# Performance work log

Hardware: AMD Instinct MI355X
Metric: run time of the kernel (lower is better)

## Reference

```python
import jax, jax.numpy as jnp
import numpy as np

BATCH, SEQ_LEN, D_MODEL = 8, 2048, 1024


def setup_inputs() -> dict:
    key = jax.random.key(0)
    ks = jax.random.split(key, 12)
    s = 0.02  # small init scale (stand-in for xavier)
    D, L = D_MODEL, SEQ_LEN
    return {
        "x": jax.random.normal(ks[0], (BATCH, L, D), jnp.float32),
        "W_B": jax.random.normal(ks[1], (D, D), jnp.float32) * s,
        "b_B": jnp.zeros((D,), jnp.float32),
        "W_C": jax.random.normal(ks[2], (D, D), jnp.float32) * s,
        "b_C": jnp.zeros((D,), jnp.float32),
        "W_d": jax.random.normal(ks[3], (D, D), jnp.float32) * s,
        "b_d": jnp.zeros((D,), jnp.float32),
        "delta_p": jax.random.normal(ks[4], (1, L, D), jnp.float32) * s,  # self.delta
        "A": jax.random.normal(ks[5], (L, D), jnp.float32) * s,
        "W_st": jax.random.normal(ks[6], (D, D), jnp.float32) * s,  # SToken fc1 Linear
        "b_st": jnp.zeros((D,), jnp.float32),
        "st_bias": jax.random.normal(ks[7], (1, 1, D), jnp.float32) * s,  # SToken bias
    }


def reference(x, W_B, b_B, W_C, b_C, W_d, b_d, delta_p, A, W_st, b_st, st_bias):
    # x: [B, L, D]
    z = jax.nn.sigmoid(x)
    B0 = x @ W_B.T + b_B          # LN_B(x)
    C = x @ W_C.T + b_C           # LN_C(x)

    # SToken: squeeze over seq, Linear -> ReLU -> Sigmoid, + bias, * x
    sq = jnp.mean(x, axis=1, keepdims=True)                    # [B, 1, D]
    sq = jax.nn.sigmoid(jax.nn.relu(sq @ W_st.T + b_st))
    T = (sq + st_bias) * x                                     # [B, L, D]

    delta = jax.nn.sigmoid(x @ W_d.T + b_d + delta_p)          # [B, L, D]
    A_ = delta * A                                             # broadcast [L, D]
    B_ = delta * B0

    # diagonal state-space recurrence: s_t = A_t * s_{t-1} + B_t * x_t; y_t = C_t * s_t + T_t
    def step(s, inputs):
        a_t, b_t, c_t, x_t, t_t = inputs                       # each [B, D]
        s = a_t * s + b_t * x_t
        y = c_t * s + t_t
        return s, y

    s0 = jnp.zeros((x.shape[0], x.shape[2]), x.dtype)
    xs = tuple(jnp.swapaxes(a, 0, 1) for a in (A_, B_, C, x, T))  # [L, B, D]
    _, ys = jax.lax.scan(step, s0, xs)
    x_out = jnp.swapaxes(ys, 0, 1) * z                         # [B, L, D]
    return x_out
```

## Files before the change

kernel.cpp:

```cpp
#include <hip/hip_runtime.h>
#include <hip/hip_bf16.h>
#include <cstdint>
#include <cstddef>

#define D_MODEL 1024
#define SEQ     2048
#define BATCH   8
#define M_TOT   (BATCH*SEQ)
#define N_TOT   (3*D_MODEL)
#define K_TOT   D_MODEL
#define KTILES  (K_TOT/64)
#define NCH     64
#define LCH     (SEQ/NCH)
#define W_UP    8

typedef unsigned short u16;
typedef __attribute__((ext_vector_type(8))) short short8;
typedef __attribute__((ext_vector_type(4))) float f32x4;

__device__ __forceinline__ u16 f2bf(float f) {
    __hip_bfloat16 h = __float2bfloat16(f);
    return __builtin_bit_cast(u16, h);
}
__device__ __forceinline__ uint packbf(float lo, float hi) {
    return (uint)f2bf(lo) | ((uint)f2bf(hi) << 16);
}
__device__ __forceinline__ float bf2f(u16 u) {
    __hip_bfloat16 h = __builtin_bit_cast(__hip_bfloat16, u);
    return __bfloat162float(h);
}
__device__ __forceinline__ float sigmoidf(float v) {
    return 1.0f / (1.0f + __expf(-v));
}
__device__ __forceinline__ void gld_lds16(const void* g, void* l) {
    __builtin_amdgcn_global_load_lds((const __attribute__((address_space(1))) void*)g,
                                     (__attribute__((address_space(3))) void*)l, 16, 0, 0);
}
__device__ __forceinline__ void wg_barrier() {
    asm volatile("" ::: "memory");
    __builtin_amdgcn_s_barrier();
    asm volatile("" ::: "memory");
}

__global__ void k_convert(const float* __restrict__ x, u16* __restrict__ xb,
                          float* __restrict__ sq,
                          const float* __restrict__ WB, const float* __restrict__ WC,
                          const float* __restrict__ Wd, u16* __restrict__ wcat,
                          const float* __restrict__ dp, const float* __restrict__ Aar,
                          uint2* __restrict__ dpA) {
    int bid = blockIdx.x;
    if (bid < 512) {
        int tblk = bid & 63, b = bid >> 6;
        int d = threadIdx.x * 4;
        size_t base = ((size_t)b * SEQ + (size_t)tblk * 32) * D_MODEL + d;
        float s0 = 0.f, s1 = 0.f, s2 = 0.f, s3 = 0.f;
        for (int t = 0; t < 32; ++t) {
            float4 v = *(const float4*)&x[base + (size_t)t * D_MODEL];
            s0 += v.x; s1 += v.y; s2 += v.z; s3 += v.w;
            ushort4 o = make_ushort4(f2bf(v.x), f2bf(v.y), f2bf(v.z), f2bf(v.w));
            *(ushort4*)&xb[base + (size_t)t * D_MODEL] = o;
        }
        atomicAdd(&sq[b * D_MODEL + d + 0], s0);
        atomicAdd(&sq[b * D_MODEL + d + 1], s1);
        atomicAdd(&sq[b * D_MODEL + d + 2], s2);
        atomicAdd(&sq[b * D_MODEL + d + 3], s3);
    } else if (bid < 3584) {
        int tg = (bid - 512) * 256 + threadIdx.x;
        size_t e0 = (size_t)tg * 4;
        int n = (int)(e0 >> 10), k0 = (int)(e0 & 1023);
        const float* W = (n < 1024) ? (WB + (size_t)n * 1024)
                       : (n < 2048) ? (WC + (size_t)(n - 1024) * 1024)
                                    : (Wd + (size_t)(n - 2048) * 1024);
        float4 v = *(const float4*)&W[k0];
        wcat[e0 + 0] = f2bf(v.x);
        wcat[e0 + 1] = f2bf(v.y);
        wcat[e0 + 2] = f2bf(v.z);
        wcat[e0 + 3] = f2bf(v.w);
    } else {
        int tg = (bid - 3584) * 256 + threadIdx.x;
        size_t e0 = (size_t)tg * 8;
        float4 d0 = *(const float4*)&dp[e0];
        float4 d1 = *(const float4*)&dp[e0 + 4];
        float4 a0 = *(const float4*)&Aar[e0];
        float4 a1 = *(const float4*)&Aar[e0 + 4];
        uint2* o = &dpA[e0 >> 1];
        o[0] = make_uint2(packbf(d0.x, d0.y), packbf(a0.x, a0.y));
        o[1] = make_uint2(packbf(d0.z, d0.w), packbf(a0.z, a0.w));
        o[2] = make_uint2(packbf(d1.x, d1.y), packbf(a1.x, a1.y));
        o[3] = make_uint2(packbf(d1.z, d1.w), packbf(a1.z, a1.w));
    }
}

__global__ void k_stoken(const float* __restrict__ sq, const float* __restrict__ Wst,
                         float* __restrict__ stacc) {
    __shared__ float s[BATCH][64];
    int nb = blockIdx.x & 3, ks = blockIdx.x >> 2;
    int k0 = ks * 64;
    for (int i = threadIdx.x; i < BATCH * 64; i += 256)
        s[i >> 6][i & 63] = sq[(i >> 6) * D_MODEL + k0 + (i & 63)] * (1.0f / SEQ);
    __syncthreads();
    int n = nb * 256 + threadIdx.x;
    const float* w = Wst + (size_t)n * D_MODEL + k0;
    float acc[BATCH] = {};
    for (int k = 0; k < 64; k += 4) {
        float4 wv = *(const float4*)&w[k];
#pragma unroll
        for (int b = 0; b < BATCH; ++b)
            acc[b] += s[b][k] * wv.x + s[b][k+1] * wv.y + s[b][k+2] * wv.z + s[b][k+3] * wv.w;
    }
#pragma unroll
    for (int b = 0; b < BATCH; ++b)
        atomicAdd(&stacc[b * D_MODEL + n], acc[b]);
}

#define HT_AL 0
#define HT_AH 1
#define HT_BL 2
#define HT_BH 3

__device__ __forceinline__ u16* ht_ptr(u16* ls, int buf, int which) {
    return ls + (size_t)(buf * 4 + which) * 8192;
}

__device__ __forceinline__ short8 ldsfrag2(const u16* ht, int R, int slot) {
    int off = R * 128 + ((slot ^ (R & 7)) << 4);
    return *(const short8*)((const char*)ht + off);
}

__device__ __forceinline__ void stage_half(const u16* __restrict__ S, u16* dst,
                                           int rowbase, int ktile, int w, int l) {
    int rsub = l >> 3;
    int scol = ((l & 7) ^ rsub) << 4;
    size_t kbyte = (size_t)ktile * 128;
#pragma unroll
    for (int j = 0; j < 2; ++j) {
        int s = 2 * w + j;
        int row = rowbase + s * 8 + rsub;
        gld_lds16((const char*)(S + (size_t)row * K_TOT) + kbyte + scol,
                  (char*)dst + s * 1024);
    }
}

template<bool SG, bool LAST>
__device__ __forceinline__ void kgroup4(const u16* __restrict__ A, const u16* __restrict__ Bm,
                                        u16* ls, int t, int i0, int n0,
                                        int wM, int wN, int r, int g, int w, int l,
                                        f32x4 acc[8][4]) {
    const int p = t & 1;
    u16* AL = ht_ptr(ls, p, HT_AL);
    u16* AH = ht_ptr(ls, p, HT_AH);
    u16* BL = ht_ptr(ls, p, HT_BL);
    u16* BH = ht_ptr(ls, p, HT_BH);
    u16* nAL = ht_ptr(ls, p ^ 1, HT_AL);
    u16* nAH = ht_ptr(ls, p ^ 1, HT_AH);
    u16* nBL = ht_ptr(ls, p ^ 1, HT_BL);
    u16* nBH = ht_ptr(ls, p ^ 1, HT_BH);
    const int RA = wM * 64 + r;
    const int RB = wN * 32 + r;

    short8 a[4][2], bl[2][2], bh[2][2];

#pragma unroll
    for (int m = 0; m < 4; ++m) {
        a[m][0] = ldsfrag2(AL, RA + m * 16, g);
        a[m][1] = ldsfrag2(AL, RA + m * 16, 4 + g);
    }
#pragma unroll
    for (int n = 0; n < 2; ++n) {
        bl[n][0] = ldsfrag2(BL, RB + n * 16, g);
        bl[n][1] = ldsfrag2(BL, RB + n * 16, 4 + g);
    }
    if (SG) stage_half(A, nAL, i0, t + 1, w, l);
    if (LAST) asm volatile("s_waitcnt vmcnt(0)" ::: "memory");
    else      asm volatile("s_waitcnt vmcnt(4)" ::: "memory");
    wg_barrier();
    __builtin_amdgcn_s_setprio(1);
#pragma unroll
    for (int m = 0; m < 4; ++m)
#pragma unroll
        for (int n = 0; n < 2; ++n)
            acc[m][n] = __builtin_amdgcn_mfma_f32_16x16x32_bf16(a[m][1], bl[n][1],
                        __builtin_amdgcn_mfma_f32_16x16x32_bf16(a[m][0], bl[n][0], acc[m][n], 0, 0, 0), 0, 0, 0);
    __builtin_amdgcn_s_setprio(0);

#pragma unroll
    for (int n = 0; n < 2; ++n) {
        bh[n][0] = ldsfrag2(BH, RB + n * 16, g);
        bh[n][1] = ldsfrag2(BH, RB + n * 16, 4 + g);
    }
    if (SG) stage_half(Bm, nBL, n0, t + 1, w, l);
    if (!LAST) asm volatile("s_waitcnt vmcnt(4)" ::: "memory");
    wg_barrier();
    __builtin_amdgcn_s_setprio(1);
#pragma unroll
    for (int m = 0; m < 4; ++m)
#pragma unroll
        for (int n = 0; n < 2; ++n)
            acc[m][2 + n] = __builtin_amdgcn_mfma_f32_16x16x32_bf16(a[m][1], bh[n][1],
                            __builtin_amdgcn_mfma_f32_16x16x32_bf16(a[m][0], bh[n][0], acc[m][2 + n], 0, 0, 0), 0, 0, 0);
    __builtin_amdgcn_s_setprio(0);

#pragma unroll
    for (int m = 0; m < 4; ++m) {
        a[m][0] = ldsfrag2(AH, RA + m * 16, g);
        a[m][1] = ldsfrag2(AH, RA + m * 16, 4 + g);
    }
    if (SG) stage_half(Bm, nBH, n0 + 128, t + 1, w, l);
    if (!LAST) asm volatile("s_waitcnt vmcnt(4)" ::: "memory");
    wg_barrier();
    __builtin_amdgcn_s_setprio(1);
#pragma unroll
    for (int m = 0; m < 4; ++m)
#pragma unroll
        for (int n = 0; n < 2; ++n)
            acc[4 + m][n] = __builtin_amdgcn_mfma_f32_16x16x32_bf16(a[m][1], bl[n][1],
                            __builtin_amdgcn_mfma_f32_16x16x32_bf16(a[m][0], bl[n][0], acc[4 + m][n], 0, 0, 0), 0, 0, 0);
    __builtin_amdgcn_s_setprio(0);

    if (SG) stage_half(A, nAH, i0 + 128, t + 1, w, l);
    if (!LAST) asm volatile("s_waitcnt vmcnt(4)" ::: "memory");
    wg_barrier();
    __builtin_amdgcn_s_setprio(1);
#pragma unroll
    for (int m = 0; m < 4; ++m)
#pragma unroll
        for (int n = 0; n < 2; ++n)
            acc[4 + m][2 + n] = __builtin_amdgcn_mfma_f32_16x16x32_bf16(a[m][1], bh[n][1],
                                __builtin_amdgcn_mfma_f32_16x16x32_bf16(a[m][0], bh[n][0], acc[4 + m][2 + n], 0, 0, 0), 0, 0, 0);
    __builtin_amdgcn_s_setprio(0);
}

__global__ __launch_bounds__(512, 2) void k_gemm(const u16* __restrict__ A,
                                                 const u16* __restrict__ Bm,
                                                 u16* __restrict__ Cout) {
    __shared__ u16 ls[8 * 8192];
    const int tid = threadIdx.x;
    const int l = tid & 63, w = tid >> 6;
    const int wM = w >> 2, wN = w & 3;
    const int r = l & 15, g = l >> 4;
    const int i0 = blockIdx.y * 256;
    const int n0 = blockIdx.x * 256;

    f32x4 acc[8][4] = {};

    stage_half(A,  ht_ptr(ls, 0, HT_AL), i0,       0, w, l);
    stage_half(Bm, ht_ptr(ls, 0, HT_BL), n0,       0, w, l);
    stage_half(Bm, ht_ptr(ls, 0, HT_BH), n0 + 128, 0, w, l);
    stage_half(A,  ht_ptr(ls, 0, HT_AH), i0 + 128, 0, w, l);
    asm volatile("s_waitcnt vmcnt(4)" ::: "memory");
    wg_barrier();

    for (int t = 0; t < KTILES - 1; ++t)
        kgroup4<true, false>(A, Bm, ls, t, i0, n0, wM, wN, r, g, w, l, acc);
    kgroup4<false, true>(A, Bm, ls, KTILES - 1, i0, n0, wM, wN, r, g, w, l, acc);

#pragma unroll
    for (int mi = 0; mi < 8; ++mi)
#pragma unroll
        for (int nj = 0; nj < 4; ++nj)
#pragma unroll
            for (int j = 0; j < 4; ++j) {
                size_t row = (size_t)(i0 + (mi >> 2) * 128 + wM * 64 + (mi & 3) * 16 + g * 4 + j);
                size_t col = (size_t)(n0 + (nj >> 1) * 128 + wN * 32 + (nj & 1) * 16 + r);
                Cout[row * N_TOT + col] = f2bf(acc[mi][nj][j]);
            }
}

__global__ void k_scan(const u16* __restrict__ xb, const u16* __restrict__ g3,
                       const uint2* __restrict__ dpA,
                       const float* __restrict__ bB, const float* __restrict__ bC,
                       const float* __restrict__ bd, const float* __restrict__ stacc,
                       const float* __restrict__ bst, const float* __restrict__ stb,
                       float* __restrict__ out) {
    int bid = blockIdx.x;
    int dblk = bid & 1, c = (bid >> 1) & (NCH - 1), b = bid >> 7;
    int d = dblk * 512 + threadIdx.x * 2;

    float2 bBv = *(const float2*)&bB[d];
    float2 bdv = *(const float2*)&bd[d];
    float2 bCv = *(const float2*)&bC[d];
    float2 sav = *(const float2*)&stacc[b * D_MODEL + d];
    float2 bstv = *(const float2*)&bst[d];
    float2 stbv = *(const float2*)&stb[d];
    float tc0 = sigmoidf(fmaxf(sav.x + bstv.x, 0.f)) + stbv.x;
    float tc1 = sigmoidf(fmaxf(sav.y + bstv.y, 0.f)) + stbv.y;

    int t0 = c * LCH;
    int tw = (c == 0) ? 0 : t0 - W_UP;
    float s0 = 0.f, s1 = 0.f;

    size_t xoff = ((size_t)b * SEQ + tw) * D_MODEL + d;
    size_t goff = ((size_t)b * SEQ + tw) * N_TOT + d;
    size_t ipa  = ((size_t)tw * D_MODEL + d) >> 1;

    for (int t = tw; t < t0; ++t) {
        uint xu = *(const uint*)&xb[xoff];
        uint gB = *(const uint*)&g3[goff];
        uint gd = *(const uint*)&g3[goff + 2048];
        uint2 pa = dpA[ipa];
        float x0 = bf2f((u16)(xu & 0xffff)), x1 = bf2f((u16)(xu >> 16));
        float b00 = bf2f((u16)(gB & 0xffff)) + bBv.x;
        float b01 = bf2f((u16)(gB >> 16)) + bBv.y;
        float de0 = sigmoidf(bf2f((u16)(gd & 0xffff)) + bdv.x + bf2f((u16)(pa.x & 0xffff)));
        float de1 = sigmoidf(bf2f((u16)(gd >> 16)) + bdv.y + bf2f((u16)(pa.x >> 16)));
        s0 = de0 * bf2f((u16)(pa.y & 0xffff)) * s0 + de0 * b00 * x0;
        s1 = de1 * bf2f((u16)(pa.y >> 16))    * s1 + de1 * b01 * x1;
        xoff += D_MODEL; goff += N_TOT; ipa += D_MODEL / 2;
    }
    for (int t = t0; t < t0 + LCH; ++t) {
        uint xu = *(const uint*)&xb[xoff];
        uint gB = *(const uint*)&g3[goff];
        uint gC = *(const uint*)&g3[goff + 1024];
        uint gd = *(const uint*)&g3[goff + 2048];
        uint2 pa = dpA[ipa];
        float x0 = bf2f((u16)(xu & 0xffff)), x1 = bf2f((u16)(xu >> 16));
        float b00 = bf2f((u16)(gB & 0xffff)) + bBv.x;
        float b01 = bf2f((u16)(gB >> 16)) + bBv.y;
        float de0 = sigmoidf(bf2f((u16)(gd & 0xffff)) + bdv.x + bf2f((u16)(pa.x & 0xffff)));
        float de1 = sigmoidf(bf2f((u16)(gd >> 16)) + bdv.y + bf2f((u16)(pa.x >> 16)));
        s0 = de0 * bf2f((u16)(pa.y & 0xffff)) * s0 + de0 * b00 * x0;
        s1 = de1 * bf2f((u16)(pa.y >> 16))    * s1 + de1 * b01 * x1;
        float c0 = bf2f((u16)(gC & 0xffff)) + bCv.x;
        float c1 = bf2f((u16)(gC >> 16)) + bCv.y;
        float y0 = (c0 * s0 + tc0 * x0) * sigmoidf(x0);
        float y1 = (c1 * s1 + tc1 * x1) * sigmoidf(x1);
        *(float2*)&out[xoff] = make_float2(y0, y1);
        xoff += D_MODEL; goff += N_TOT; ipa += D_MODEL / 2;
    }
}

extern "C" void kernel_launch(void* const* d_in, const int* in_sizes, int n_in,
                              void* d_out, int out_size, void* d_ws, size_t ws_size,
                              hipStream_t stream) {
    const float* x    = (const float*)d_in[0];
    const float* W_B  = (const float*)d_in[1];
    const float* b_B  = (const float*)d_in[2];
    const float* W_C  = (const float*)d_in[3];
    const float* b_C  = (const float*)d_in[4];
    const float* W_d  = (const float*)d_in[5];
    const float* b_d  = (const float*)d_in[6];
    const float* dp   = (const float*)d_in[7];
    const float* Aar  = (const float*)d_in[8];
    const float* W_st = (const float*)d_in[9];
    const float* b_st = (const float*)d_in[10];
    const float* stb  = (const float*)d_in[11];
    float* out = (float*)d_out;

    char* ws = (char*)d_ws;
    u16* xb    = (u16*)ws;   ws += (size_t)M_TOT * K_TOT * 2;
    u16* wcat  = (u16*)ws;   ws += (size_t)N_TOT * K_TOT * 2;
    u16* g3    = (u16*)ws;   ws += (size_t)M_TOT * N_TOT * 2;
    uint2* dpA = (uint2*)ws; ws += (size_t)SEQ * D_MODEL / 2 * 8;
    float* sq    = (float*)ws; ws += (size_t)BATCH * D_MODEL * 4;
    float* stacc = (float*)ws; ws += (size_t)BATCH * D_MODEL * 4;

    hipMemsetAsync(sq, 0, (size_t)2 * BATCH * D_MODEL * 4, stream);
    k_convert<<<4608, 256, 0, stream>>>(x, xb, sq, W_B, W_C, W_d, wcat, dp, Aar, dpA);
    k_stoken<<<64, 256, 0, stream>>>(sq, W_st, stacc);
    k_gemm<<<dim3(N_TOT / 256, M_TOT / 256), 512, 0, stream>>>(xb, wcat, g3);
    k_scan<<<1024, 256, 0, stream>>>(xb, g3, dpA, b_B, b_C, b_d,
                                     stacc, b_st, stb, out);
}
```

Measured before the change: 182.8 us.

## Fold SToken projection into GEMM launch and issue next-tile loads earlier

```diff
diff --git a/kernel.cpp b/kernel.cpp
--- a/kernel.cpp
+++ b/kernel.cpp
@@ -13,6 +13,7 @@
 #define NCH     64
 #define LCH     (SEQ/NCH)
 #define W_UP    8
+#define GEMM_BLKS (M_TOT/256 * N_TOT/256)
 
 typedef unsigned short u16;
 typedef __attribute__((ext_vector_type(8))) short short8;
@@ -91,28 +92,6 @@
     }
 }
 
-__global__ void k_stoken(const float* __restrict__ sq, const float* __restrict__ Wst,
-                         float* __restrict__ stacc) {
-    __shared__ float s[BATCH][64];
-    int nb = blockIdx.x & 3, ks = blockIdx.x >> 2;
-    int k0 = ks * 64;
-    for (int i = threadIdx.x; i < BATCH * 64; i += 256)
-        s[i >> 6][i & 63] = sq[(i >> 6) * D_MODEL + k0 + (i & 63)] * (1.0f / SEQ);
-    __syncthreads();
-    int n = nb * 256 + threadIdx.x;
-    const float* w = Wst + (size_t)n * D_MODEL + k0;
-    float acc[BATCH] = {};
-    for (int k = 0; k < 64; k += 4) {
-        float4 wv = *(const float4*)&w[k];
-#pragma unroll
-        for (int b = 0; b < BATCH; ++b)
-            acc[b] += s[b][k] * wv.x + s[b][k+1] * wv.y + s[b][k+2] * wv.z + s[b][k+3] * wv.w;
-    }
-#pragma unroll
-    for (int b = 0; b < BATCH; ++b)
-        atomicAdd(&stacc[b * D_MODEL + n], acc[b]);
-}
-
 #define HT_AL 0
 #define HT_AH 1
 #define HT_BL 2
@@ -160,6 +139,7 @@
 
     short8 a[4][2], bl[2][2], bh[2][2];
 
+    if (SG) stage_half(A, nAL, i0, t + 1, w, l);
 #pragma unroll
     for (int m = 0; m < 4; ++m) {
         a[m][0] = ldsfrag2(AL, RA + m * 16, g);
@@ -170,7 +150,6 @@
         bl[n][0] = ldsfrag2(BL, RB + n * 16, g);
         bl[n][1] = ldsfrag2(BL, RB + n * 16, 4 + g);
     }
-    if (SG) stage_half(A, nAL, i0, t + 1, w, l);
     if (LAST) asm volatile("s_waitcnt vmcnt(0)" ::: "memory");
     else      asm volatile("s_waitcnt vmcnt(4)" ::: "memory");
     wg_barrier();
@@ -183,12 +162,12 @@
                         __builtin_amdgcn_mfma_f32_16x16x32_bf16(a[m][0], bl[n][0], acc[m][n], 0, 0, 0), 0, 0, 0);
     __builtin_amdgcn_s_setprio(0);
 
+    if (SG) stage_half(Bm, nBL, n0, t + 1, w, l);
 #pragma unroll
     for (int n = 0; n < 2; ++n) {
         bh[n][0] = ldsfrag2(BH, RB + n * 16, g);
         bh[n][1] = ldsfrag2(BH, RB + n * 16, 4 + g);
     }
-    if (SG) stage_half(Bm, nBL, n0, t + 1, w, l);
     if (!LAST) asm volatile("s_waitcnt vmcnt(4)" ::: "memory");
     wg_barrier();
     __builtin_amdgcn_s_setprio(1);
@@ -200,12 +179,12 @@
                             __builtin_amdgcn_mfma_f32_16x16x32_bf16(a[m][0], bh[n][0], acc[m][2 + n], 0, 0, 0), 0, 0, 0);
     __builtin_amdgcn_s_setprio(0);
 
+    if (SG) stage_half(Bm, nBH, n0 + 128, t + 1, w, l);
 #pragma unroll
     for (int m = 0; m < 4; ++m) {
         a[m][0] = ldsfrag2(AH, RA + m * 16, g);
         a[m][1] = ldsfrag2(AH, RA + m * 16, 4 + g);
     }
-    if (SG) stage_half(Bm, nBH, n0 + 128, t + 1, w, l);
     if (!LAST) asm volatile("s_waitcnt vmcnt(4)" ::: "memory");
     wg_barrier();
     __builtin_amdgcn_s_setprio(1);
@@ -232,14 +211,44 @@
 
 __global__ __launch_bounds__(512, 2) void k_gemm(const u16* __restrict__ A,
                                                  const u16* __restrict__ Bm,
-                                                 u16* __restrict__ Cout) {
+                                                 u16* __restrict__ Cout,
+                                                 const float* __restrict__ sq,
+                                                 const float* __restrict__ Wst,
+                                                 float* __restrict__ stacc) {
     __shared__ u16 ls[8 * 8192];
+    const int bid = blockIdx.x;
     const int tid = threadIdx.x;
+
+    if (bid >= GEMM_BLKS) {
+        float* s = (float*)ls;
+        int sb = bid - GEMM_BLKS;
+        int nb = sb & 1, ks = sb >> 1;
+        int k0 = ks * 64;
+        if (tid < BATCH * 64)
+            s[tid] = sq[(tid >> 6) * D_MODEL + k0 + (tid & 63)] * (1.0f / SEQ);
+        __syncthreads();
+        int n = nb * 512 + tid;
+        const float* wp = Wst + (size_t)n * D_MODEL + k0;
+        float acc[BATCH] = {};
+        for (int k = 0; k < 64; k += 4) {
+            float4 wv = *(const float4*)&wp[k];
+#pragma unroll
+            for (int b = 0; b < BATCH; ++b) {
+                const float* sb_ = s + b * 64 + k;
+                acc[b] += sb_[0] * wv.x + sb_[1] * wv.y + sb_[2] * wv.z + sb_[3] * wv.w;
+            }
+        }
+#pragma unroll
+        for (int b = 0; b < BATCH; ++b)
+            atomicAdd(&stacc[b * D_MODEL + n], acc[b]);
+        return;
+    }
+
     const int l = tid & 63, w = tid >> 6;
     const int wM = w >> 2, wN = w & 3;
     const int r = l & 15, g = l >> 4;
-    const int i0 = blockIdx.y * 256;
-    const int n0 = blockIdx.x * 256;
+    const int i0 = (bid / 12) * 256;
+    const int n0 = (bid % 12) * 256;
 
     f32x4 acc[8][4] = {};
 
@@ -356,8 +365,7 @@
 
     hipMemsetAsync(sq, 0, (size_t)2 * BATCH * D_MODEL * 4, stream);
     k_convert<<<4608, 256, 0, stream>>>(x, xb, sq, W_B, W_C, W_d, wcat, dp, Aar, dpA);
-    k_stoken<<<64, 256, 0, stream>>>(sq, W_st, stacc);
-    k_gemm<<<dim3(N_TOT / 256, M_TOT / 256), 512, 0, stream>>>(xb, wcat, g3);
+    k_gemm<<<GEMM_BLKS + 32, 512, 0, stream>>>(xb, wcat, g3, sq, W_st, stacc);
     k_scan<<<1024, 256, 0, stream>>>(xb, g3, dpA, b_B, b_C, b_d,
                                      stacc, b_st, stb, out);
 }
```

Measured after the change: 183.9 us. No clear change (+0.6%).
